# Kernel tuning notes

Measured on AMD Instinct MI355X. Metric: run time of the kernel, lower is better.

## Reference

```python
import jax, jax.numpy as jnp
import numpy as np

B, L, C, H, DK, MAXR = 2, 2048, 256, 8, 32, 7
NEG = jnp.float32(-2**32 + 1)


def _rel_tab(L, maxR):
    # |i-j| with log2 bucketing beyond maxR, clipped to [0, 2*maxR]
    i = jnp.arange(L)
    d = jnp.abs(i[:, None] - i[None, :]).astype(jnp.float32)
    d = jnp.where(d > maxR, maxR + jnp.log2(jnp.maximum(d - maxR, 1.0)), d)
    return jnp.clip(d, 0, 2 * maxR).astype(jnp.int32)  # [L, L]


def setup_inputs() -> dict:
    key = jax.random.key(0)
    ks = jax.random.split(key, 14)
    s = 0.02
    return {
        "qx": jax.random.normal(ks[0], (B, L, C), jnp.float32),
        "kx": jax.random.normal(ks[1], (B, L, C), jnp.float32),
        "vx": jax.random.normal(ks[2], (B, L, C), jnp.float32),
        "preScores": jax.random.normal(ks[3], (B, H, L, L), jnp.float32),
        "maskPAD": jnp.ones((B, L, L), jnp.int32),
        "WQ_w": jax.random.normal(ks[4], (C, H * DK), jnp.float32) * s,
        "WQ_b": jnp.zeros((H * DK,), jnp.float32),
        "WK_w": jax.random.normal(ks[5], (C, H * DK), jnp.float32) * s,
        "WK_b": jnp.zeros((H * DK,), jnp.float32),
        "WV_w": jax.random.normal(ks[6], (C, H * DK), jnp.float32) * s,
        "WV_b": jnp.zeros((H * DK,), jnp.float32),
        "WO_w": jax.random.normal(ks[7], (H * DK, C), jnp.float32) * s,
        "WO_b": jnp.zeros((C,), jnp.float32),
        "embK": jax.random.normal(ks[8], (2 * MAXR + 1, H), jnp.float32),
        "embB": jax.random.normal(ks[9], (2 * MAXR + 1, H), jnp.float32),
    }


def reference(qx, kx, vx, preScores, maskPAD,
              WQ_w, WQ_b, WK_w, WK_b, WV_w, WV_b, WO_w, WO_b, embK, embB):
    q = (qx @ WQ_w + WQ_b).reshape(B, L, H, DK)
    k = (kx @ WK_w + WK_b).reshape(B, L, H, DK)
    v = (vx @ WV_w + WV_b).reshape(B, L, H, DK)
    scores = jnp.einsum('blhd,bmhd->bhlm', q, k) / jnp.float32(np.sqrt(DK))
    tab = _rel_tab(L, MAXR)                       # [L, L] int32
    kb = jnp.transpose(embK[tab], (2, 0, 1))[None]  # [1, H, L, L]
    bb = jnp.transpose(embB[tab], (2, 0, 1))[None]
    scores = scores * kb + bb + preScores
    scores = jnp.where(maskPAD[:, None, :, :] == 0, NEG, scores)
    alpha = jax.nn.softmax(scores, axis=3)        # dropout = identity (eval)
    z = jnp.einsum('bhlm,bmhd->blhd', alpha, v).reshape(B, L, H * DK)
    z = z @ WO_w + WO_b
    return (z, scores)
```

## Files before the change

### kernel.cpp

```cpp
#include <hip/hip_runtime.h>
#include <hip/hip_bf16.h>
#include <math.h>

typedef __bf16 bf16;
typedef __bf16 bf16x8 __attribute__((ext_vector_type(8)));
typedef __bf16 bf16x4 __attribute__((ext_vector_type(4)));
typedef float  f32x4  __attribute__((ext_vector_type(4)));

#define NB 2
#define NL 2048
#define NC 256
#define NH 8
#define NDK 32
#define SCALE 0.17677669529663687f
#define NEGV  -4294967296.0f

__global__ __launch_bounds__(256) void proj_kernel(
    const float* __restrict__ qx, const float* __restrict__ kx, const float* __restrict__ vx,
    const float* __restrict__ Wq, const float* __restrict__ bq,
    const float* __restrict__ Wk, const float* __restrict__ bk,
    const float* __restrict__ Wv, const float* __restrict__ bv,
    bf16* __restrict__ qo, bf16* __restrict__ ko, bf16* __restrict__ vto)
{
    const int mode = blockIdx.z;
    const float* X    = (mode == 0) ? qx : (mode == 1) ? kx : vx;
    const float* W    = (mode == 0) ? Wq : (mode == 1) ? Wk : Wv;
    const float* bias = (mode == 0) ? bq : (mode == 1) ? bk : bv;

    __shared__ float As[64][33];
    __shared__ float Bs[32][65];

    const int tid = threadIdx.x;
    const int tx = tid & 15, ty = tid >> 4;
    const int m0 = blockIdx.x * 64, n0 = blockIdx.y * 64;

    float acc[4][4] = {{0.f}};

    for (int k0 = 0; k0 < NC; k0 += 32) {
        const int ar = tid >> 2, ac = (tid & 3) << 3;
        const float4 a0 = *(const float4*)(X + (size_t)(m0 + ar) * NC + k0 + ac);
        const float4 a1 = *(const float4*)(X + (size_t)(m0 + ar) * NC + k0 + ac + 4);
        const int br = tid >> 3, bc = (tid & 7) << 3;
        const float4 b0 = *(const float4*)(W + (size_t)(k0 + br) * NC + n0 + bc);
        const float4 b1 = *(const float4*)(W + (size_t)(k0 + br) * NC + n0 + bc + 4);
        __syncthreads();
        As[ar][ac+0]=a0.x; As[ar][ac+1]=a0.y; As[ar][ac+2]=a0.z; As[ar][ac+3]=a0.w;
        As[ar][ac+4]=a1.x; As[ar][ac+5]=a1.y; As[ar][ac+6]=a1.z; As[ar][ac+7]=a1.w;
        Bs[br][bc+0]=b0.x; Bs[br][bc+1]=b0.y; Bs[br][bc+2]=b0.z; Bs[br][bc+3]=b0.w;
        Bs[br][bc+4]=b1.x; Bs[br][bc+5]=b1.y; Bs[br][bc+6]=b1.z; Bs[br][bc+7]=b1.w;
        __syncthreads();
        #pragma unroll
        for (int kk = 0; kk < 32; ++kk) {
            float av[4], bw[4];
            #pragma unroll
            for (int r = 0; r < 4; ++r) av[r] = As[ty*4+r][kk];
            #pragma unroll
            for (int c = 0; c < 4; ++c) bw[c] = Bs[kk][tx*4+c];
            #pragma unroll
            for (int r = 0; r < 4; ++r)
                #pragma unroll
                for (int c = 0; c < 4; ++c)
                    acc[r][c] = fmaf(av[r], bw[c], acc[r][c]);
        }
    }

    #pragma unroll
    for (int r = 0; r < 4; ++r) {
        const int row = m0 + ty*4 + r;
        const int bb_ = row >> 11, ll = row & (NL - 1);
        #pragma unroll
        for (int c = 0; c < 4; ++c) {
            const int col = n0 + tx*4 + c;
            const float v = acc[r][c] + bias[col];
            const int hh = col >> 5, d = col & 31;
            if (mode == 0)
                qo[(((size_t)bb_*NH + hh)*NL + ll)*NDK + d] = (bf16)v;
            else if (mode == 1)
                ko[(((size_t)bb_*NH + hh)*NL + ll)*NDK + d] = (bf16)v;
            else
                vto[(((size_t)bb_*NH + hh)*NDK + d)*NL + ll] = (bf16)v;
        }
    }
}

__global__ __launch_bounds__(256) void out_gemm_kernel(
    const float* __restrict__ Z, const float* __restrict__ W,
    const float* __restrict__ bias, float* __restrict__ out)
{
    __shared__ float As[64][33];
    __shared__ float Bs[32][65];

    const int tid = threadIdx.x;
    const int tx = tid & 15, ty = tid >> 4;
    const int m0 = blockIdx.x * 64, n0 = blockIdx.y * 64;

    float acc[4][4] = {{0.f}};

    for (int k0 = 0; k0 < NC; k0 += 32) {
        const int ar = tid >> 2, ac = (tid & 3) << 3;
        const float4 a0 = *(const float4*)(Z + (size_t)(m0 + ar) * NC + k0 + ac);
        const float4 a1 = *(const float4*)(Z + (size_t)(m0 + ar) * NC + k0 + ac + 4);
        const int br = tid >> 3, bc = (tid & 7) << 3;
        const float4 b0 = *(const float4*)(W + (size_t)(k0 + br) * NC + n0 + bc);
        const float4 b1 = *(const float4*)(W + (size_t)(k0 + br) * NC + n0 + bc + 4);
        __syncthreads();
        As[ar][ac+0]=a0.x; As[ar][ac+1]=a0.y; As[ar][ac+2]=a0.z; As[ar][ac+3]=a0.w;
        As[ar][ac+4]=a1.x; As[ar][ac+5]=a1.y; As[ar][ac+6]=a1.z; As[ar][ac+7]=a1.w;
        Bs[br][bc+0]=b0.x; Bs[br][bc+1]=b0.y; Bs[br][bc+2]=b0.z; Bs[br][bc+3]=b0.w;
        Bs[br][bc+4]=b1.x; Bs[br][bc+5]=b1.y; Bs[br][bc+6]=b1.z; Bs[br][bc+7]=b1.w;
        __syncthreads();
        #pragma unroll
        for (int kk = 0; kk < 32; ++kk) {
            float av[4], bw[4];
            #pragma unroll
            for (int r = 0; r < 4; ++r) av[r] = As[ty*4+r][kk];
            #pragma unroll
            for (int c = 0; c < 4; ++c) bw[c] = Bs[kk][tx*4+c];
            #pragma unroll
            for (int r = 0; r < 4; ++r)
                #pragma unroll
                for (int c = 0; c < 4; ++c)
                    acc[r][c] = fmaf(av[r], bw[c], acc[r][c]);
        }
    }

    #pragma unroll
    for (int r = 0; r < 4; ++r) {
        const int row = m0 + ty*4 + r;
        #pragma unroll
        for (int c = 0; c < 4; ++c) {
            const int col = n0 + tx*4 + c;
            out[(size_t)row * NC + col] = acc[r][c] + bias[col];
        }
    }
}

__global__ __launch_bounds__(256) void attn_kernel(
    const bf16* __restrict__ q, const bf16* __restrict__ k, const bf16* __restrict__ vt,
    const float* __restrict__ preScores, const int* __restrict__ maskPAD,
    const float* __restrict__ embK, const float* __restrict__ embB,
    float* __restrict__ scores_out, float* __restrict__ zbuf)
{
    const int b  = blockIdx.z, h = blockIdx.y;
    const int i0 = blockIdx.x * 64;
    const int tid = threadIdx.x;
    const int lane = tid & 63, w = tid >> 6;
    const int l15 = lane & 15, g = lane >> 4;

    __shared__ __align__(16) bf16 Qs[64][40];
    __shared__ __align__(16) bf16 Ks[64][40];
    __shared__ __align__(16) bf16 Vts[32][72];
    __shared__ __align__(16) bf16 Ps[4][16][72];
    __shared__ float2 kbb[NL];

    for (int d = tid; d < NL; d += 256) {
        const float fd = (float)d;
        float t = (d > 7) ? (7.0f + log2f(fd - 7.0f)) : fd;
        int idx = (int)t; idx = idx > 14 ? 14 : idx;
        kbb[d] = make_float2(embK[idx * NH + h], embB[idx * NH + h]);
    }

    const size_t bh = (size_t)b * NH + h;
    {
        const int r = tid >> 2, c = (tid & 3) << 3;
        const uint4 qv = *(const uint4*)(q + (bh * NL + i0 + r) * NDK + c);
        *(uint4*)&Qs[r][c] = qv;
    }
    __syncthreads();

    const bf16x8 bQ = *(const bf16x8*)&Qs[(w << 4) | l15][g * 8];

    f32x4 oF0 = {0.f, 0.f, 0.f, 0.f};
    f32x4 oF1 = {0.f, 0.f, 0.f, 0.f};
    float m_run = -INFINITY, l_run = 0.f;
    const f32x4 zf = {0.f, 0.f, 0.f, 0.f};

    const int i_row = i0 + (w << 4) + l15;
    const float* preRow  = preScores  + (bh * NL + i_row) * (size_t)NL;
    const int*   maskRow = maskPAD    + ((size_t)b * NL + i_row) * (size_t)NL;
    float*       scoreRow = scores_out + (bh * NL + i_row) * (size_t)NL;

    for (int j0 = 0; j0 < NL; j0 += 64) {
        const int kr = tid >> 2, kc = (tid & 3) << 3;
        const uint4 kv = *(const uint4*)(k + (bh * NL + j0 + kr) * NDK + kc);
        const int vr = tid >> 3, vc = (tid & 7) << 3;
        const uint4 vv = *(const uint4*)(vt + (bh * NDK + vr) * NL + j0 + vc);
        __syncthreads();
        *(uint4*)&Ks[kr][kc]  = kv;
        *(uint4*)&Vts[vr][vc] = vv;
        __syncthreads();

        f32x4 sf[4];
        #pragma unroll
        for (int tj = 0; tj < 4; ++tj) {
            const bf16x8 aK = *(const bf16x8*)&Ks[(tj << 4) | l15][g * 8];
            sf[tj] = __builtin_amdgcn_mfma_f32_16x16x32_bf16(aK, bQ, zf, 0, 0, 0);
        }

        float pv[4][4];
        float pmax = -INFINITY;
        #pragma unroll
        for (int tj = 0; tj < 4; ++tj) {
            const int jb = j0 + (tj << 4) + (g << 2);
            const float4 pre4 = *(const float4*)(preRow + jb);
            const int4   mk4  = *(const int4*)(maskRow + jb);
            float4 out4;
            #pragma unroll
            for (int r = 0; r < 4; ++r) {
                const int j = jb + r;
                int dd = i_row - j; dd = dd < 0 ? -dd : dd;
                const float2 kb2 = kbb[dd];
                float sv = sf[tj][r] * SCALE;
                sv = sv * kb2.x + kb2.y + (&pre4.x)[r];
                if ((&mk4.x)[r] == 0) sv = NEGV;
                (&out4.x)[r] = sv;
                pv[tj][r] = sv;
                pmax = fmaxf(pmax, sv);
            }
            *(float4*)(scoreRow + jb) = out4;
        }
        pmax = fmaxf(pmax, __shfl_xor(pmax, 16, 64));
        pmax = fmaxf(pmax, __shfl_xor(pmax, 32, 64));

        const float mn = fmaxf(m_run, pmax);
        const float sc = __expf(m_run - mn);
        m_run = mn;
        float rsum = 0.f;
        #pragma unroll
        for (int tj = 0; tj < 4; ++tj)
            #pragma unroll
            for (int r = 0; r < 4; ++r) {
                pv[tj][r] = __expf(pv[tj][r] - mn);
                rsum += pv[tj][r];
            }
        rsum += __shfl_xor(rsum, 16, 64);
        rsum += __shfl_xor(rsum, 32, 64);
        l_run = l_run * sc + rsum;

        #pragma unroll
        for (int r = 0; r < 4; ++r) {
            const float scr = __shfl(sc, 20 * g + r, 64);
            oF0[r] *= scr;
            oF1[r] *= scr;
        }

        #pragma unroll
        for (int tj = 0; tj < 4; ++tj) {
            bf16x4 pk;
            pk[0] = (bf16)pv[tj][0];
            pk[1] = (bf16)pv[tj][1];
            pk[2] = (bf16)pv[tj][2];
            pk[3] = (bf16)pv[tj][3];
            *(bf16x4*)&Ps[w][l15][(tj << 4) | (g << 2)] = pk;
        }
        asm volatile("s_waitcnt lgkmcnt(0)" ::: "memory");

        #pragma unroll
        for (int cc = 0; cc < 2; ++cc) {
            const bf16x8 aP  = *(const bf16x8*)&Ps[w][l15][cc * 32 + g * 8];
            const bf16x8 bV0 = *(const bf16x8*)&Vts[l15][cc * 32 + g * 8];
            const bf16x8 bV1 = *(const bf16x8*)&Vts[16 + l15][cc * 32 + g * 8];
            oF0 = __builtin_amdgcn_mfma_f32_16x16x32_bf16(aP, bV0, oF0, 0, 0, 0);
            oF1 = __builtin_amdgcn_mfma_f32_16x16x32_bf16(aP, bV1, oF1, 0, 0, 0);
        }
    }

    const float linv = 1.0f / l_run;
    #pragma unroll
    for (int r = 0; r < 4; ++r) {
        const float li = __shfl(linv, 20 * g + r, 64);
        const int i = i0 + (w << 4) + (g << 2) + r;
        float* zr = zbuf + ((size_t)b * NL + i) * (size_t)(NH * NDK) + h * NDK;
        zr[l15]      = oF0[r] * li;
        zr[16 + l15] = oF1[r] * li;
    }
}

extern "C" void kernel_launch(void* const* d_in, const int* in_sizes, int n_in,
                              void* d_out, int out_size, void* d_ws, size_t ws_size,
                              hipStream_t stream) {
    (void)in_sizes; (void)n_in; (void)out_size; (void)ws_size;

    const float* qx        = (const float*)d_in[0];
    const float* kx        = (const float*)d_in[1];
    const float* vx        = (const float*)d_in[2];
    const float* preScores = (const float*)d_in[3];
    const int*   maskPAD   = (const int*)  d_in[4];
    const float* WQ_w      = (const float*)d_in[5];
    const float* WQ_b      = (const float*)d_in[6];
    const float* WK_w      = (const float*)d_in[7];
    const float* WK_b      = (const float*)d_in[8];
    const float* WV_w      = (const float*)d_in[9];
    const float* WV_b      = (const float*)d_in[10];
    const float* WO_w      = (const float*)d_in[11];
    const float* WO_b      = (const float*)d_in[12];
    const float* embK      = (const float*)d_in[13];
    const float* embB      = (const float*)d_in[14];

    char* ws = (char*)d_ws;
    bf16*  qb   = (bf16*)(ws);
    bf16*  kb   = (bf16*)(ws + (2u << 20));
    bf16*  vtb  = (bf16*)(ws + (4u << 20));
    float* zbuf = (float*)(ws + (6u << 20));

    float* z_out      = (float*)d_out;
    float* scores_out = (float*)d_out + (size_t)NB * NL * NC;

    proj_kernel<<<dim3(64, 4, 3), 256, 0, stream>>>(
        qx, kx, vx, WQ_w, WQ_b, WK_w, WK_b, WV_w, WV_b, qb, kb, vtb);

    attn_kernel<<<dim3(NL / 64, NH, NB), 256, 0, stream>>>(
        qb, kb, vtb, preScores, maskPAD, embK, embB, scores_out, zbuf);

    out_gemm_kernel<<<dim3(64, 4), 256, 0, stream>>>(zbuf, WO_w, WO_b, z_out);
}
```

Before: 255.6 us.

## Split attention over key chunks with a combine pass, plus software prefetch

Splits the key dimension into four chunks, launching four times as many attention blocks, each writing partial outputs plus running max and sum, which a new combine kernel merges. The attention loop register-prefetches the next K/V, preScores and mask tiles, uses nontemporal loads and stores for the large score streams, and computes the relative-position bucket with clz against a 15-entry table instead of a 2048-entry LDS table. The output GEMM uses 32-row tiles for more blocks. The goal is more parallelism and latency hiding on this memory-bound kernel, at the cost of an extra launch and partial-result traffic.

```diff
diff --git a/kernel.cpp b/kernel.cpp
--- a/kernel.cpp
+++ b/kernel.cpp
@@ -6,12 +6,16 @@
 typedef __bf16 bf16x8 __attribute__((ext_vector_type(8)));
 typedef __bf16 bf16x4 __attribute__((ext_vector_type(4)));
 typedef float  f32x4  __attribute__((ext_vector_type(4)));
+typedef int    i32x4  __attribute__((ext_vector_type(4)));
 
 #define NB 2
 #define NL 2048
 #define NC 256
 #define NH 8
 #define NDK 32
+#define JSPLIT 4
+#define JCHUNK (NL / JSPLIT)
+#define JTILES (JCHUNK / 64)
 #define SCALE 0.17677669529663687f
 #define NEGV  -4294967296.0f
 
@@ -87,37 +91,35 @@
     const float* __restrict__ Z, const float* __restrict__ W,
     const float* __restrict__ bias, float* __restrict__ out)
 {
-    __shared__ float As[64][33];
+    __shared__ float As[32][33];
     __shared__ float Bs[32][65];
 
     const int tid = threadIdx.x;
     const int tx = tid & 15, ty = tid >> 4;
-    const int m0 = blockIdx.x * 64, n0 = blockIdx.y * 64;
-
-    float acc[4][4] = {{0.f}};
+    const int m0 = blockIdx.x * 32, n0 = blockIdx.y * 64;
+
+    float acc[2][4] = {{0.f}};
 
     for (int k0 = 0; k0 < NC; k0 += 32) {
-        const int ar = tid >> 2, ac = (tid & 3) << 3;
+        const int ar = tid >> 3, ac = (tid & 7) << 2;
         const float4 a0 = *(const float4*)(Z + (size_t)(m0 + ar) * NC + k0 + ac);
-        const float4 a1 = *(const float4*)(Z + (size_t)(m0 + ar) * NC + k0 + ac + 4);
         const int br = tid >> 3, bc = (tid & 7) << 3;
         const float4 b0 = *(const float4*)(W + (size_t)(k0 + br) * NC + n0 + bc);
         const float4 b1 = *(const float4*)(W + (size_t)(k0 + br) * NC + n0 + bc + 4);
         __syncthreads();
         As[ar][ac+0]=a0.x; As[ar][ac+1]=a0.y; As[ar][ac+2]=a0.z; As[ar][ac+3]=a0.w;
-        As[ar][ac+4]=a1.x; As[ar][ac+5]=a1.y; As[ar][ac+6]=a1.z; As[ar][ac+7]=a1.w;
         Bs[br][bc+0]=b0.x; Bs[br][bc+1]=b0.y; Bs[br][bc+2]=b0.z; Bs[br][bc+3]=b0.w;
         Bs[br][bc+4]=b1.x; Bs[br][bc+5]=b1.y; Bs[br][bc+6]=b1.z; Bs[br][bc+7]=b1.w;
         __syncthreads();
         #pragma unroll
         for (int kk = 0; kk < 32; ++kk) {
-            float av[4], bw[4];
-            #pragma unroll
-            for (int r = 0; r < 4; ++r) av[r] = As[ty*4+r][kk];
+            float av[2], bw[4];
+            av[0] = As[ty*2+0][kk];
+            av[1] = As[ty*2+1][kk];
             #pragma unroll
             for (int c = 0; c < 4; ++c) bw[c] = Bs[kk][tx*4+c];
             #pragma unroll
-            for (int r = 0; r < 4; ++r)
+            for (int r = 0; r < 2; ++r)
                 #pragma unroll
                 for (int c = 0; c < 4; ++c)
                     acc[r][c] = fmaf(av[r], bw[c], acc[r][c]);
@@ -125,8 +127,8 @@
     }
 
     #pragma unroll
-    for (int r = 0; r < 4; ++r) {
-        const int row = m0 + ty*4 + r;
+    for (int r = 0; r < 2; ++r) {
+        const int row = m0 + ty*2 + r;
         #pragma unroll
         for (int c = 0; c < 4; ++c) {
             const int col = n0 + tx*4 + c;
@@ -135,60 +137,67 @@
     }
 }
 
-__global__ __launch_bounds__(256) void attn_kernel(
+__global__ __launch_bounds__(256, 4) void attn_kernel(
     const bf16* __restrict__ q, const bf16* __restrict__ k, const bf16* __restrict__ vt,
     const float* __restrict__ preScores, const int* __restrict__ maskPAD,
     const float* __restrict__ embK, const float* __restrict__ embB,
-    float* __restrict__ scores_out, float* __restrict__ zbuf)
+    float* __restrict__ scores_out, float* __restrict__ zp, float2* __restrict__ ml)
 {
-    const int b  = blockIdx.z, h = blockIdx.y;
-    const int i0 = blockIdx.x * 64;
+    const int h  = blockIdx.x & (NH - 1);
+    const int i0 = (blockIdx.x >> 3) << 6;
+    const int js = blockIdx.y;
+    const int b  = blockIdx.z;
     const int tid = threadIdx.x;
     const int lane = tid & 63, w = tid >> 6;
     const int l15 = lane & 15, g = lane >> 4;
 
-    __shared__ __align__(16) bf16 Qs[64][40];
     __shared__ __align__(16) bf16 Ks[64][40];
     __shared__ __align__(16) bf16 Vts[32][72];
     __shared__ __align__(16) bf16 Ps[4][16][72];
-    __shared__ float2 kbb[NL];
-
-    for (int d = tid; d < NL; d += 256) {
-        const float fd = (float)d;
-        float t = (d > 7) ? (7.0f + log2f(fd - 7.0f)) : fd;
-        int idx = (int)t; idx = idx > 14 ? 14 : idx;
-        kbb[d] = make_float2(embK[idx * NH + h], embB[idx * NH + h]);
-    }
+    __shared__ float2 tab[16];
+
+    if (tid < 15) tab[tid] = make_float2(embK[tid * NH + h], embB[tid * NH + h]);
 
     const size_t bh = (size_t)b * NH + h;
-    {
-        const int r = tid >> 2, c = (tid & 3) << 3;
-        const uint4 qv = *(const uint4*)(q + (bh * NL + i0 + r) * NDK + c);
-        *(uint4*)&Qs[r][c] = qv;
-    }
-    __syncthreads();
-
-    const bf16x8 bQ = *(const bf16x8*)&Qs[(w << 4) | l15][g * 8];
+    const int i_row = i0 + (w << 4) + l15;
+    const bf16x8 bQ = *(const bf16x8*)(q + (bh * NL + i_row) * NDK + g * 8);
+
+    const int kr = tid >> 2, kc = (tid & 3) << 3;
+    const int vr = tid >> 3, vc = (tid & 7) << 3;
+    const bf16* kbase = k  + (bh * NL + kr) * NDK + kc;
+    const bf16* vbase = vt + (bh * NDK + vr) * NL + vc;
+
+    const float* preRow   = preScores  + (bh * NL + i_row) * (size_t)NL;
+    const int*   maskRow  = maskPAD    + ((size_t)b * NL + i_row) * (size_t)NL;
+    float*       scoreRow = scores_out + (bh * NL + i_row) * (size_t)NL;
 
     f32x4 oF0 = {0.f, 0.f, 0.f, 0.f};
     f32x4 oF1 = {0.f, 0.f, 0.f, 0.f};
     float m_run = -INFINITY, l_run = 0.f;
     const f32x4 zf = {0.f, 0.f, 0.f, 0.f};
 
-    const int i_row = i0 + (w << 4) + l15;
-    const float* preRow  = preScores  + (bh * NL + i_row) * (size_t)NL;
-    const int*   maskRow = maskPAD    + ((size_t)b * NL + i_row) * (size_t)NL;
-    float*       scoreRow = scores_out + (bh * NL + i_row) * (size_t)NL;
-
-    for (int j0 = 0; j0 < NL; j0 += 64) {
-        const int kr = tid >> 2, kc = (tid & 3) << 3;
-        const uint4 kv = *(const uint4*)(k + (bh * NL + j0 + kr) * NDK + kc);
-        const int vr = tid >> 3, vc = (tid & 7) << 3;
-        const uint4 vv = *(const uint4*)(vt + (bh * NDK + vr) * NL + j0 + vc);
-        __syncthreads();
-        *(uint4*)&Ks[kr][kc]  = kv;
-        *(uint4*)&Vts[vr][vc] = vv;
-        __syncthreads();
+    const int jc0 = js * JCHUNK;
+
+    uint4 kv_c = *(const uint4*)(kbase + (size_t)jc0 * NDK);
+    uint4 vv_c = *(const uint4*)(vbase + jc0);
+    f32x4 pre_c[4]; i32x4 mk_c[4];
+    #pragma unroll
+    for (int tj = 0; tj < 4; ++tj) {
+        const int jb = jc0 + (tj << 4) + (g << 2);
+        pre_c[tj] = __builtin_nontemporal_load((const f32x4*)(preRow + jb));
+        mk_c[tj]  = *(const i32x4*)(maskRow + jb);
+    }
+
+    #pragma unroll
+    for (int jt = 0; jt < JTILES; ++jt) {
+        const int j0 = jc0 + jt * 64;
+
+        asm volatile("s_waitcnt lgkmcnt(0)" ::: "memory");
+        __builtin_amdgcn_s_barrier();
+        *(uint4*)&Ks[kr][kc]  = kv_c;
+        *(uint4*)&Vts[vr][vc] = vv_c;
+        asm volatile("s_waitcnt lgkmcnt(0)" ::: "memory");
+        __builtin_amdgcn_s_barrier();
 
         f32x4 sf[4];
         #pragma unroll
@@ -197,28 +206,47 @@
             sf[tj] = __builtin_amdgcn_mfma_f32_16x16x32_bf16(aK, bQ, zf, 0, 0, 0);
         }
 
-        float pv[4][4];
+        uint4 kv_n, vv_n;
+        if (jt + 1 < JTILES) {
+            kv_n = *(const uint4*)(kbase + (size_t)(j0 + 64) * NDK);
+            vv_n = *(const uint4*)(vbase + (j0 + 64));
+        }
+
         float pmax = -INFINITY;
         #pragma unroll
         for (int tj = 0; tj < 4; ++tj) {
             const int jb = j0 + (tj << 4) + (g << 2);
-            const float4 pre4 = *(const float4*)(preRow + jb);
-            const int4   mk4  = *(const int4*)(maskRow + jb);
-            float4 out4;
+            f32x4 out4;
             #pragma unroll
             for (int r = 0; r < 4; ++r) {
                 const int j = jb + r;
                 int dd = i_row - j; dd = dd < 0 ? -dd : dd;
-                const float2 kb2 = kbb[dd];
+                int idx = dd;
+                if (dd > 7) {
+                    idx = 38 - __clz(dd - 7);
+                    idx = idx > 14 ? 14 : idx;
+                }
+                const float2 kb2 = tab[idx];
                 float sv = sf[tj][r] * SCALE;
-                sv = sv * kb2.x + kb2.y + (&pre4.x)[r];
-                if ((&mk4.x)[r] == 0) sv = NEGV;
-                (&out4.x)[r] = sv;
-                pv[tj][r] = sv;
+                sv = sv * kb2.x + kb2.y + pre_c[tj][r];
+                if (mk_c[tj][r] == 0) sv = NEGV;
+                out4[r] = sv;
+                sf[tj][r] = sv;
                 pmax = fmaxf(pmax, sv);
             }
-            *(float4*)(scoreRow + jb) = out4;
-        }
+            __builtin_nontemporal_store(out4, (f32x4*)(scoreRow + jb));
+        }
+
+        f32x4 pre_n[4]; i32x4 mk_n[4];
+        if (jt + 1 < JTILES) {
+            #pragma unroll
+            for (int tj = 0; tj < 4; ++tj) {
+                const int jb = j0 + 64 + (tj << 4) + (g << 2);
+                pre_n[tj] = __builtin_nontemporal_load((const f32x4*)(preRow + jb));
+                mk_n[tj]  = *(const i32x4*)(maskRow + jb);
+            }
+        }
+
         pmax = fmaxf(pmax, __shfl_xor(pmax, 16, 64));
         pmax = fmaxf(pmax, __shfl_xor(pmax, 32, 64));
 
@@ -230,8 +258,9 @@
         for (int tj = 0; tj < 4; ++tj)
             #pragma unroll
             for (int r = 0; r < 4; ++r) {
-                pv[tj][r] = __expf(pv[tj][r] - mn);
-                rsum += pv[tj][r];
+                const float e = __expf(sf[tj][r] - mn);
+                sf[tj][r] = e;
+                rsum += e;
             }
         rsum += __shfl_xor(rsum, 16, 64);
         rsum += __shfl_xor(rsum, 32, 64);
@@ -247,10 +276,10 @@
         #pragma unroll
         for (int tj = 0; tj < 4; ++tj) {
             bf16x4 pk;
-            pk[0] = (bf16)pv[tj][0];
-            pk[1] = (bf16)pv[tj][1];
-            pk[2] = (bf16)pv[tj][2];
-            pk[3] = (bf16)pv[tj][3];
+            pk[0] = (bf16)sf[tj][0];
+            pk[1] = (bf16)sf[tj][1];
+            pk[2] = (bf16)sf[tj][2];
+            pk[3] = (bf16)sf[tj][3];
             *(bf16x4*)&Ps[w][l15][(tj << 4) | (g << 2)] = pk;
         }
         asm volatile("s_waitcnt lgkmcnt(0)" ::: "memory");
@@ -263,17 +292,51 @@
             oF0 = __builtin_amdgcn_mfma_f32_16x16x32_bf16(aP, bV0, oF0, 0, 0, 0);
             oF1 = __builtin_amdgcn_mfma_f32_16x16x32_bf16(aP, bV1, oF1, 0, 0, 0);
         }
-    }
-
-    const float linv = 1.0f / l_run;
+
+        if (jt + 1 < JTILES) {
+            kv_c = kv_n; vv_c = vv_n;
+            #pragma unroll
+            for (int t = 0; t < 4; ++t) { pre_c[t] = pre_n[t]; mk_c[t] = mk_n[t]; }
+        }
+    }
+
     #pragma unroll
     for (int r = 0; r < 4; ++r) {
-        const float li = __shfl(linv, 20 * g + r, 64);
         const int i = i0 + (w << 4) + (g << 2) + r;
-        float* zr = zbuf + ((size_t)b * NL + i) * (size_t)(NH * NDK) + h * NDK;
-        zr[l15]      = oF0[r] * li;
-        zr[16 + l15] = oF1[r] * li;
-    }
+        float* zr = zp + ((bh * JSPLIT + js) * (size_t)NL + i) * NDK;
+        zr[l15]      = oF0[r];
+        zr[16 + l15] = oF1[r];
+    }
+    if (g == 0)
+        ml[(bh * JSPLIT + js) * (size_t)NL + i_row] = make_float2(m_run, l_run);
+}
+
+__global__ __launch_bounds__(256) void combine_kernel(
+    const float* __restrict__ zp, const float2* __restrict__ ml, float* __restrict__ zbuf)
+{
+    const int gid = blockIdx.x * 256 + threadIdx.x;
+    const int d   = gid & (NDK - 1);
+    const int row = gid >> 5;
+    const int i   = row & (NL - 1);
+    const int bh  = row >> 11;
+    const int h   = bh & (NH - 1), b = bh >> 3;
+
+    float m[JSPLIT], l[JSPLIT];
+    float M = -INFINITY;
+    #pragma unroll
+    for (int js = 0; js < JSPLIT; ++js) {
+        const float2 t = ml[((size_t)bh * JSPLIT + js) * NL + i];
+        m[js] = t.x; l[js] = t.y;
+        M = fmaxf(M, t.x);
+    }
+    float L = 0.f, zs = 0.f;
+    #pragma unroll
+    for (int js = 0; js < JSPLIT; ++js) {
+        const float e = __expf(m[js] - M);
+        L += l[js] * e;
+        zs = fmaf(zp[(((size_t)bh * JSPLIT + js) * NL + i) * NDK + d], e, zs);
+    }
+    zbuf[((size_t)b * NL + i) * NC + h * NDK + d] = zs / L;
 }
 
 extern "C" void kernel_launch(void* const* d_in, const int* in_sizes, int n_in,
@@ -298,10 +361,12 @@
     const float* embB      = (const float*)d_in[14];
 
     char* ws = (char*)d_ws;
-    bf16*  qb   = (bf16*)(ws);
-    bf16*  kb   = (bf16*)(ws + (2u << 20));
-    bf16*  vtb  = (bf16*)(ws + (4u << 20));
-    float* zbuf = (float*)(ws + (6u << 20));
+    bf16*   qb   = (bf16*)(ws);
+    bf16*   kb   = (bf16*)(ws + (2u << 20));
+    bf16*   vtb  = (bf16*)(ws + (4u << 20));
+    float*  zbuf = (float*)(ws + (6u << 20));
+    float*  zp   = (float*)(ws + (10u << 20));
+    float2* mlb  = (float2*)(ws + (26u << 20));
 
     float* z_out      = (float*)d_out;
     float* scores_out = (float*)d_out + (size_t)NB * NL * NC;
@@ -309,8 +374,10 @@
     proj_kernel<<<dim3(64, 4, 3), 256, 0, stream>>>(
         qx, kx, vx, WQ_w, WQ_b, WK_w, WK_b, WV_w, WV_b, qb, kb, vtb);
 
-    attn_kernel<<<dim3(NL / 64, NH, NB), 256, 0, stream>>>(
-        qb, kb, vtb, preScores, maskPAD, embK, embB, scores_out, zbuf);
-
-    out_gemm_kernel<<<dim3(64, 4), 256, 0, stream>>>(zbuf, WO_w, WO_b, z_out);
-}
+    attn_kernel<<<dim3((NL / 64) * NH, JSPLIT, NB), 256, 0, stream>>>(
+        qb, kb, vtb, preScores, maskPAD, embK, embB, scores_out, zp, mlb);
+
+    combine_kernel<<<dim3((NB * NH * NL * NDK) / 256), 256, 0, stream>>>(zp, mlb, zbuf);
+
+    out_gemm_kernel<<<dim3(NB * NL / 32, 4), 256, 0, stream>>>(zbuf, WO_w, WO_b, z_out);
+}
```

Measured after the change: 236.6 us. 7.4% less time.
